# Optimization experiments

Measured on AMD Instinct MI355X. Metric: run time of the kernel, lower is better.

The kernel has to match this reference:

```python
import jax, jax.numpy as jnp
import numpy as np

SIGMA = 0.3
EPS = 1e-8  # torch CosineSimilarity eps
LOG_SQRT_2PI = float(0.5 * np.log(2.0 * np.pi))


def setup_inputs() -> dict:
    key = jax.random.key(0)
    k1, k2 = jax.random.split(key)
    Ex = jax.random.normal(k1, (8192, 256), dtype=jnp.float32)
    Ey = jax.random.normal(k2, (8192, 256), dtype=jnp.float32)
    return {"Ex": Ex, "Ey": Ey}


def reference(Ex, Ey):
    # cosine similarity: normalize rows (clamped norms), then dot -> [n, m]
    xn = Ex / jnp.maximum(jnp.linalg.norm(Ex, axis=-1, keepdims=True), EPS)
    yn = Ey / jnp.maximum(jnp.linalg.norm(Ey, axis=-1, keepdims=True), EPS)
    M = jnp.einsum('nd,md->nm', xn, yn)
    # Normal(loc=1, scale=sigma).log_prob
    z = (M - 1.0) / SIGMA
    logp = -0.5 * z * z - jnp.log(jnp.asarray(SIGMA, M.dtype)) - LOG_SQRT_2PI
    # C = -(exp(logp) * logp); row-wise min over y-tokens -> [n]
    C = -jnp.exp(logp) * logp
    return jnp.min(C, axis=-1)
```

## Files before the change

### kernel.cpp

```cpp
#include <hip/hip_runtime.h>
#include <hip/hip_bf16.h>

typedef unsigned short u16;
typedef __attribute__((ext_vector_type(8))) short short8;
typedef __attribute__((ext_vector_type(4))) float floatx4;

#define NROWS 8192
#define DIM 256

__device__ __forceinline__ void atomicMinFloat(float* addr, float val) {
    if (val >= 0.0f) {
        atomicMin((int*)addr, __float_as_int(val));
    } else {
        atomicMax((unsigned int*)addr, __float_as_uint(val));
    }
}

__device__ __forceinline__ u16 f32_to_bf16_rne(float x) {
    unsigned int u = __float_as_uint(x);
    unsigned int r = (u + 0x7fffu + ((u >> 16) & 1u)) >> 16;
    return (u16)r;
}

__device__ __forceinline__ float c_of_m(float m) {
    const float INV_SIG = 1.0f / 0.3f;
    const float KC = 0.28503427f;
    float z = (m - 1.0f) * INV_SIG;
    float logp = fmaf(-0.5f * z, z, KC);
    return -logp * __expf(logp);
}

__device__ __forceinline__ void load16(const u16* g, u16* l) {
    __builtin_amdgcn_global_load_lds(
        (__attribute__((address_space(1))) void*)g,
        (__attribute__((address_space(3))) void*)l, 16, 0, 0);
}

__global__ __launch_bounds__(256) void normalize_kernel(const float* __restrict__ Ex,
                                                        const float* __restrict__ Ey,
                                                        u16* __restrict__ Xs,
                                                        u16* __restrict__ Ys,
                                                        float* __restrict__ out) {
    const int t = threadIdx.x;
    const int ln = t & 63;
    const int row = blockIdx.x * 4 + (t >> 6);
    const float* src = (blockIdx.y == 0) ? Ex : Ey;
    u16* dst = (blockIdx.y == 0) ? Xs : Ys;

    float4 v = *(const float4*)(src + (size_t)row * DIM + ln * 4);
    float s = fmaf(v.x, v.x, fmaf(v.y, v.y, fmaf(v.z, v.z, v.w * v.w)));
    #pragma unroll
    for (int m = 32; m >= 1; m >>= 1) s += __shfl_xor(s, m, 64);
    float inv = 1.0f / fmaxf(sqrtf(s), 1e-8f);

    ushort4 o;
    o.x = f32_to_bf16_rne(v.x * inv);
    o.y = f32_to_bf16_rne(v.y * inv);
    o.z = f32_to_bf16_rne(v.z * inv);
    o.w = f32_to_bf16_rne(v.w * inv);

    const int p = row >> 4;
    const int lm = row & 15;
    const int kt = ln >> 3;
    const int lq = (ln >> 1) & 3;
    const int j4 = (ln & 1) * 4;
    const size_t off = ((size_t)((p * 8 + kt) * 64 + lq * 16 + lm)) * 8 + j4;
    *(ushort4*)(dst + off) = o;

    if (blockIdx.y == 0 && ln == 0) out[row] = __uint_as_float(0x7f800000u);
}

__global__ void __launch_bounds__(512, 2)
gemm_min_kernel(const u16* __restrict__ Xs,
                const u16* __restrict__ Ys,
                float* __restrict__ out) {
    __shared__ u16 Bs[2][32 * 512];

    const int tid = threadIdx.x;
    const int w = tid >> 6;
    const int lane = tid & 63;
    const int lq = lane >> 4;
    const int lm = lane & 15;

    const int b = blockIdx.x;
    const int rowStart = (b & 15) * 512;
    const int rowPan0 = (b & 15) * 32 + w * 4;
    const u16* ybase = Ys + (size_t)((b >> 4) * 32) * 4096;

    auto stageB = [&](int buf, const u16* yb) {
        #pragma unroll
        for (int i = 0; i < 4; ++i) {
            const int u = w * 4 + i;
            load16(yb + (u >> 3) * 4096 + (u & 7) * 512 + lane * 8,
                   &Bs[buf][u * 512]);
        }
    };

    short8 a[4][8];
    auto loadA = [&](int kt) {
        #pragma unroll
        for (int rg = 0; rg < 4; ++rg)
            a[rg][kt] = *(const short8*)(
                Xs + ((size_t)(rowPan0 + rg) * 8 + kt) * 512 + lane * 8);
    };

    floatx4 mn4[4], mx4[4];
    #pragma unroll
    for (int rg = 0; rg < 4; ++rg) {
        mn4[rg] = (floatx4){3.4e38f, 3.4e38f, 3.4e38f, 3.4e38f};
        mx4[rg] = (floatx4){-3.4e38f, -3.4e38f, -3.4e38f, -3.4e38f};
    }

    floatx4 acc[4][4];
    const floatx4 FZ = (floatx4){0.0f, 0.0f, 0.0f, 0.0f};

    auto compute = [&](int buf) {
        #pragma unroll
        for (int kt = 0; kt < 8; ++kt) {
            short8 bf[4];
            #pragma unroll
            for (int cg = 0; cg < 4; ++cg)
                bf[cg] = *(const short8*)(&Bs[buf][(cg * 8 + kt) * 512 + lane * 8]);
            __builtin_amdgcn_s_setprio(1);
            if (kt == 0) {
                #pragma unroll
                for (int cg = 0; cg < 4; ++cg)
                    #pragma unroll
                    for (int rg = 0; rg < 4; ++rg)
                        acc[rg][cg] = __builtin_amdgcn_mfma_f32_16x16x32_bf16(
                            a[rg][0], bf[cg], FZ, 0, 0, 0);
            } else {
                #pragma unroll
                for (int cg = 0; cg < 4; ++cg)
                    #pragma unroll
                    for (int rg = 0; rg < 4; ++rg)
                        acc[rg][cg] = __builtin_amdgcn_mfma_f32_16x16x32_bf16(
                            a[rg][kt], bf[cg], acc[rg][cg], 0, 0, 0);
            }
            __builtin_amdgcn_s_setprio(0);
        }
    };
    auto fold = [&]() {
        #pragma unroll
        for (int rg = 0; rg < 4; ++rg)
            #pragma unroll
            for (int cg = 0; cg < 4; ++cg)
                #pragma unroll
                for (int r = 0; r < 4; ++r) {
                    float m = acc[rg][cg][r];
                    mn4[rg][r] = fminf(mn4[rg][r], m);
                    mx4[rg][r] = fmaxf(mx4[rg][r], m);
                }
    };

    stageB(0, ybase);
    loadA(0);
    loadA(1);
    __syncthreads();
    stageB(1, ybase + 16384);
    loadA(2); loadA(3); loadA(4); loadA(5); loadA(6); loadA(7);
    compute(0);
    fold();
    ybase += 16384;

    #pragma unroll 1
    for (int ct = 1; ct < 8; ++ct) {
        const int buf = ct & 1;
        __syncthreads();
        if (ct < 7)
            stageB(buf ^ 1, ybase + 16384);
        compute(buf);
        fold();
        ybase += 16384;
    }

    #pragma unroll
    for (int rg = 0; rg < 4; ++rg) {
        #pragma unroll
        for (int r = 0; r < 4; ++r) {
            float mn = mn4[rg][r];
            float mx = mx4[rg][r];
            #pragma unroll
            for (int mofs = 1; mofs < 16; mofs <<= 1) {
                mn = fminf(mn, __shfl_xor(mn, mofs, 64));
                mx = fmaxf(mx, __shfl_xor(mx, mofs, 64));
            }
            if (lm == 0) {
                float cmin = fminf(c_of_m(mn), c_of_m(mx));
                int row = rowStart + w * 64 + rg * 16 + lq * 4 + r;
                atomicMinFloat(&out[row], cmin);
            }
        }
    }
}

extern "C" void kernel_launch(void* const* d_in, const int* in_sizes, int n_in,
                              void* d_out, int out_size, void* d_ws, size_t ws_size,
                              hipStream_t stream) {
    const float* Ex = (const float*)d_in[0];
    const float* Ey = (const float*)d_in[1];
    float* out = (float*)d_out;
    u16* Xs = (u16*)d_ws;
    u16* Ys = Xs + (size_t)NROWS * DIM;

    hipLaunchKernelGGL(normalize_kernel, dim3(NROWS / 4, 2), dim3(256), 0, stream,
                       Ex, Ey, Xs, Ys, out);
    hipLaunchKernelGGL(gemm_min_kernel, dim3(16 * 16), dim3(512), 0, stream,
                       Xs, Ys, out);
}
```

Before: 96.77 us.

## Drop LDS staging of B tiles and remap blocks for L2 locality

Removes the double-buffered LDS staging of Y tiles with global_load_lds. Every wave now reads its B fragments directly from global memory, relying on L2/cache reuse, and a bare s_barrier keeps the waves of a block in lockstep. The block index is also remapped so neighbouring blocks share row tiles and column groups, which should improve cache hit rates. Every wave in the block loads the same B data separately, so cache traffic rises and global load latency is no longer hidden by a prefetch buffer.

```diff
diff --git a/kernel.cpp b/kernel.cpp
--- a/kernel.cpp
+++ b/kernel.cpp
@@ -28,12 +28,6 @@
     float z = (m - 1.0f) * INV_SIG;
     float logp = fmaf(-0.5f * z, z, KC);
     return -logp * __expf(logp);
-}
-
-__device__ __forceinline__ void load16(const u16* g, u16* l) {
-    __builtin_amdgcn_global_load_lds(
-        (__attribute__((address_space(1))) void*)g,
-        (__attribute__((address_space(3))) void*)l, 16, 0, 0);
 }
 
 __global__ __launch_bounds__(256) void normalize_kernel(const float* __restrict__ Ex,
@@ -74,27 +68,21 @@
 gemm_min_kernel(const u16* __restrict__ Xs,
                 const u16* __restrict__ Ys,
                 float* __restrict__ out) {
-    __shared__ u16 Bs[2][32 * 512];
-
     const int tid = threadIdx.x;
     const int w = tid >> 6;
     const int lane = tid & 63;
     const int lq = lane >> 4;
     const int lm = lane & 15;
 
-    const int b = blockIdx.x;
-    const int rowStart = (b & 15) * 512;
-    const int rowPan0 = (b & 15) * 32 + w * 4;
-    const u16* ybase = Ys + (size_t)((b >> 4) * 32) * 4096;
+    const int i = blockIdx.x;
+    const int x = i & 7;
+    const int jj = i >> 3;
+    const int rt = (x & 3) * 4 + (jj & 3);
+    const int cgrp = (x >> 2) * 8 + (jj >> 2);
 
-    auto stageB = [&](int buf, const u16* yb) {
-        #pragma unroll
-        for (int i = 0; i < 4; ++i) {
-            const int u = w * 4 + i;
-            load16(yb + (u >> 3) * 4096 + (u & 7) * 512 + lane * 8,
-                   &Bs[buf][u * 512]);
-        }
-    };
+    const int rowStart = rt * 512;
+    const int rowPan0 = rt * 32 + w * 4;
+    const u16* ybase = Ys + (size_t)cgrp * 32 * 4096;
 
     short8 a[4][8];
     auto loadA = [&](int kt) {
@@ -103,6 +91,8 @@
             a[rg][kt] = *(const short8*)(
                 Xs + ((size_t)(rowPan0 + rg) * 8 + kt) * 512 + lane * 8);
     };
+    loadA(0); loadA(1); loadA(2); loadA(3);
+    loadA(4); loadA(5); loadA(6); loadA(7);
 
     floatx4 mn4[4], mx4[4];
     #pragma unroll
@@ -114,13 +104,15 @@
     floatx4 acc[4][4];
     const floatx4 FZ = (floatx4){0.0f, 0.0f, 0.0f, 0.0f};
 
-    auto compute = [&](int buf) {
+    #pragma unroll 1
+    for (int ct = 0; ct < 8; ++ct) {
+        if (ct) __builtin_amdgcn_s_barrier();
         #pragma unroll
         for (int kt = 0; kt < 8; ++kt) {
             short8 bf[4];
             #pragma unroll
             for (int cg = 0; cg < 4; ++cg)
-                bf[cg] = *(const short8*)(&Bs[buf][(cg * 8 + kt) * 512 + lane * 8]);
+                bf[cg] = *(const short8*)(ybase + cg * 4096 + kt * 512 + lane * 8);
             __builtin_amdgcn_s_setprio(1);
             if (kt == 0) {
                 #pragma unroll
@@ -139,8 +131,6 @@
             }
             __builtin_amdgcn_s_setprio(0);
         }
-    };
-    auto fold = [&]() {
         #pragma unroll
         for (int rg = 0; rg < 4; ++rg)
             #pragma unroll
@@ -151,26 +141,6 @@
                     mn4[rg][r] = fminf(mn4[rg][r], m);
                     mx4[rg][r] = fmaxf(mx4[rg][r], m);
                 }
-    };
-
-    stageB(0, ybase);
-    loadA(0);
-    loadA(1);
-    __syncthreads();
-    stageB(1, ybase + 16384);
-    loadA(2); loadA(3); loadA(4); loadA(5); loadA(6); loadA(7);
-    compute(0);
-    fold();
-    ybase += 16384;
-
-    #pragma unroll 1
-    for (int ct = 1; ct < 8; ++ct) {
-        const int buf = ct & 1;
-        __syncthreads();
-        if (ct < 7)
-            stageB(buf ^ 1, ybase + 16384);
-        compute(buf);
-        fold();
         ybase += 16384;
     }
 
```

After: 101.6 us. +5.0%, slower.

## Use 1024-thread blocks with 2 row groups per wave and swizzled tile mapping

Applied to the files above, without the earlier changes.

Doubles the block to 16 waves, each computing 2 row-groups of 16 instead of 4, which halves per-wave accumulator and A-fragment registers and should allow higher occupancy. Block indices are remapped so that neighbouring blocks share row and column tiles, aiming at better L2 reuse. The s_setprio hints around the MFMA loop are removed. The cost is fewer MFMAs per wave between barriers and more waves contending at each __syncthreads.

```diff
diff --git a/kernel.cpp b/kernel.cpp
--- a/kernel.cpp
+++ b/kernel.cpp
@@ -70,7 +70,7 @@
     if (blockIdx.y == 0 && ln == 0) out[row] = __uint_as_float(0x7f800000u);
 }
 
-__global__ void __launch_bounds__(512, 2)
+__global__ void __launch_bounds__(1024, 4)
 gemm_min_kernel(const u16* __restrict__ Xs,
                 const u16* __restrict__ Ys,
                 float* __restrict__ out) {
@@ -82,36 +82,38 @@
     const int lq = lane >> 4;
     const int lm = lane & 15;
 
-    const int b = blockIdx.x;
-    const int rowStart = (b & 15) * 512;
-    const int rowPan0 = (b & 15) * 32 + w * 4;
-    const u16* ybase = Ys + (size_t)((b >> 4) * 32) * 4096;
-
-    auto stageB = [&](int buf, const u16* yb) {
-        #pragma unroll
-        for (int i = 0; i < 4; ++i) {
-            const int u = w * 4 + i;
-            load16(yb + (u >> 3) * 4096 + (u & 7) * 512 + lane * 8,
-                   &Bs[buf][u * 512]);
-        }
-    };
-
-    short8 a[4][8];
+    const int i = blockIdx.x;
+    const int x = i & 7;
+    const int jj = i >> 3;
+    const int rt = (x & 3) * 4 + (jj & 3);
+    const int cgrp = (x >> 2) * 8 + (jj >> 2);
+
+    const int rowStart = rt * 512;
+    const int rowPan0 = rt * 32 + w * 2;
+    const u16* ybase = Ys + (size_t)cgrp * 32 * 4096;
+
+    auto stage1 = [&](int buf, const u16* yb, int iu) {
+        const int u = w * 2 + iu;
+        load16(yb + (u >> 3) * 4096 + (u & 7) * 512 + lane * 8,
+               &Bs[buf][u * 512]);
+    };
+
+    short8 a[2][8];
     auto loadA = [&](int kt) {
         #pragma unroll
-        for (int rg = 0; rg < 4; ++rg)
+        for (int rg = 0; rg < 2; ++rg)
             a[rg][kt] = *(const short8*)(
                 Xs + ((size_t)(rowPan0 + rg) * 8 + kt) * 512 + lane * 8);
     };
 
-    floatx4 mn4[4], mx4[4];
+    floatx4 mn4[2], mx4[2];
     #pragma unroll
-    for (int rg = 0; rg < 4; ++rg) {
+    for (int rg = 0; rg < 2; ++rg) {
         mn4[rg] = (floatx4){3.4e38f, 3.4e38f, 3.4e38f, 3.4e38f};
         mx4[rg] = (floatx4){-3.4e38f, -3.4e38f, -3.4e38f, -3.4e38f};
     }
 
-    floatx4 acc[4][4];
+    floatx4 acc[2][4];
     const floatx4 FZ = (floatx4){0.0f, 0.0f, 0.0f, 0.0f};
 
     auto compute = [&](int buf) {
@@ -121,28 +123,26 @@
             #pragma unroll
             for (int cg = 0; cg < 4; ++cg)
                 bf[cg] = *(const short8*)(&Bs[buf][(cg * 8 + kt) * 512 + lane * 8]);
-            __builtin_amdgcn_s_setprio(1);
             if (kt == 0) {
                 #pragma unroll
                 for (int cg = 0; cg < 4; ++cg)
                     #pragma unroll
-                    for (int rg = 0; rg < 4; ++rg)
+                    for (int rg = 0; rg < 2; ++rg)
                         acc[rg][cg] = __builtin_amdgcn_mfma_f32_16x16x32_bf16(
                             a[rg][0], bf[cg], FZ, 0, 0, 0);
             } else {
                 #pragma unroll
                 for (int cg = 0; cg < 4; ++cg)
                     #pragma unroll
-                    for (int rg = 0; rg < 4; ++rg)
+                    for (int rg = 0; rg < 2; ++rg)
                         acc[rg][cg] = __builtin_amdgcn_mfma_f32_16x16x32_bf16(
                             a[rg][kt], bf[cg], acc[rg][cg], 0, 0, 0);
             }
-            __builtin_amdgcn_s_setprio(0);
         }
     };
     auto fold = [&]() {
         #pragma unroll
-        for (int rg = 0; rg < 4; ++rg)
+        for (int rg = 0; rg < 2; ++rg)
             #pragma unroll
             for (int cg = 0; cg < 4; ++cg)
                 #pragma unroll
@@ -153,11 +153,10 @@
                 }
     };
 
-    stageB(0, ybase);
-    loadA(0);
-    loadA(1);
+    stage1(0, ybase, 0); stage1(0, ybase, 1);
+    loadA(0); loadA(1);
     __syncthreads();
-    stageB(1, ybase + 16384);
+    stage1(1, ybase + 16384, 0); stage1(1, ybase + 16384, 1);
     loadA(2); loadA(3); loadA(4); loadA(5); loadA(6); loadA(7);
     compute(0);
     fold();
@@ -168,14 +167,14 @@
         const int buf = ct & 1;
         __syncthreads();
         if (ct < 7)
-            stageB(buf ^ 1, ybase + 16384);
+            stage1(buf ^ 1, ybase + 16384, 0), stage1(buf ^ 1, ybase + 16384, 1);
         compute(buf);
         fold();
         ybase += 16384;
     }
 
     #pragma unroll
-    for (int rg = 0; rg < 4; ++rg) {
+    for (int rg = 0; rg < 2; ++rg) {
         #pragma unroll
         for (int r = 0; r < 4; ++r) {
             float mn = mn4[rg][r];
@@ -187,7 +186,7 @@
             }
             if (lm == 0) {
                 float cmin = fminf(c_of_m(mn), c_of_m(mx));
-                int row = rowStart + w * 64 + rg * 16 + lq * 4 + r;
+                int row = rowStart + w * 32 + rg * 16 + lq * 4 + r;
                 atomicMinFloat(&out[row], cmin);
             }
         }
@@ -205,6 +204,6 @@
 
     hipLaunchKernelGGL(normalize_kernel, dim3(NROWS / 4, 2), dim3(256), 0, stream,
                        Ex, Ey, Xs, Ys, out);
-    hipLaunchKernelGGL(gemm_min_kernel, dim3(16 * 16), dim3(512), 0, stream,
+    hipLaunchKernelGGL(gemm_min_kernel, dim3(16 * 16), dim3(1024), 0, stream,
                        Xs, Ys, out);
 }
```

Result: faster. 94.82 us (-2.0%).
